# Kernel tuning notes

Measured on AMD Instinct MI355X. Metric: run time of the kernel, lower is better.

## Reference

```python
import jax, jax.numpy as jnp
import numpy as np
from jax import lax

N, L, C_IN, NOISE_C, COMP, NC = 256, 512, 514, 112, 16, 2
MAIN_IN = NOISE_C + COMP  # 128
FEAT = NC * 4 * L         # 4096

def _conv1d(x, w, b, pad):
    # x [N,C,L], w [O,I,K]
    y = lax.conv_general_dilated(x, w, (1,), [(pad, pad)], dimension_numbers=('NCH', 'OIH', 'NCH'))
    return y + b[None, :, None]

def _bn(x, g, b):
    # BatchNorm1d, training mode: biased batch stats over (N, L)
    m = x.mean(axis=(0, 2), keepdims=True)
    v = x.var(axis=(0, 2), keepdims=True)
    return (x - m) * lax.rsqrt(v + 1e-5) * g[None, :, None] + b[None, :, None]

def _lrelu(x):
    return jnp.where(x >= 0, x, 0.2 * x)

def _pos_encode(length, dim):
    j = np.arange(dim)
    div = 1.0 / np.power(10000.0, 2 * (j[:, None] // 2) / dim)   # [dim,1]
    ang = np.arange(length)[None, :] * div                       # [dim,length]
    ang = np.where((j % 2 == 0)[:, None], np.sin(ang), np.cos(ang))
    return jnp.asarray(ang[None], jnp.float32)                   # [1,dim,length]

def _assemble(circle_prob, slider_prob):
    # Vectorized run-length label expansion equivalent to the per-sample python while-loop.
    # circle_prob [N, L/2, 2], slider_prob [N, L/4, 2] -> [N, L, 3]
    n, B = slider_prob.shape[0], slider_prob.shape[1]
    c = jnp.argmax(circle_prob, -1)
    s = jnp.argmax(slider_prob, -1)
    zc = jnp.zeros(circle_prob.shape[:-1] + (1,), circle_prob.dtype)
    zs = jnp.zeros(slider_prob.shape[:-1] + (1,), slider_prob.dtype)
    cp3 = jnp.concatenate([circle_prob, zc], -1)                                   # insert 0 at class 2
    sp3 = jnp.concatenate([slider_prob[..., :1], zs, slider_prob[..., 1:]], -1)    # insert 0 at class 1
    pad100 = jnp.array([1., 0., 0.], cp3.dtype)
    pad001 = jnp.array([0., 0., 1.], cp3.dtype)
    bidx = jnp.arange(B)[None, :]
    # slider-body blocks: slider run continues and not cut by sequence end
    body = (s == 1) & (bidx < B - 1)
    prev_body = jnp.concatenate([jnp.zeros((n, 1), bool), body[:, :-1]], 1)
    # tail block ends a slider run (either run stops, or boundary block)
    tail = ((s == 1) & (bidx == B - 1)) | ((s == 0) & prev_body)
    # circle emission for each half-step: prob row if predicted circle else pad
    cr0 = jnp.where((c == 1)[..., None], cp3, pad100).reshape(n, B, 2, 3)
    bodyE = body[..., None]
    row0 = jnp.where((body | tail)[..., None], sp3, cr0[:, :, 0, :])
    row1 = jnp.where(bodyE, pad001, pad100)
    row2 = jnp.where(bodyE, pad001, cr0[:, :, 1, :])
    row3 = jnp.where(bodyE, pad001, pad100)
    return jnp.stack([row0, row1, row2, row3], 2).reshape(n, 4 * B, 3)

def _forward(noise, cond_data, gumbel_u, ext_w1, ext_b1, ext_w2, ext_b2, ext_bn_g, ext_bn_b,
             m_w1, m_b1, m_w2, m_b2, m_bn_g, m_bn_b, lin_w, lin_b, circ_w, circ_b, slid_w, slid_b):
    # FeatureExtractor
    x = cond_data.transpose(0, 2, 1)                      # [N, 514, L]
    x = _lrelu(_conv1d(x, ext_w1, ext_b1, 0))             # [N, 32, L]
    cond = _bn(_conv1d(x, ext_w2, ext_b2, 1), ext_bn_g, ext_bn_b)  # [N, 16, L]
    gen_in = jnp.concatenate([cond, noise.transpose(0, 2, 1)], 1) + _pos_encode(L, MAIN_IN)  # [N,128,L]
    h = _lrelu(_conv1d(gen_in, m_w1, m_b1, 3))            # [N, 32, L]
    h = _lrelu(_bn(_conv1d(h, m_w2, m_b2, 1), m_bn_g, m_bn_b))     # [N, 8, L]
    flat = _lrelu(h.reshape(h.shape[0], -1) @ lin_w + lin_b)       # [N, 4096]
    circle_prob = (flat @ circ_w + circ_b).reshape(-1, L // 2, NC)
    slider_prob = (flat @ slid_w + slid_b).reshape(-1, L // 4, NC)
    out = _assemble(circle_prob, slider_prob)             # [N, L, 3]
    # gumbel_softmax(hard=True, tau=1)
    g = -jnp.log(-jnp.log(gumbel_u + 1e-10) + 1e-10)
    logits = out + g
    y_soft = jax.nn.softmax(logits, -1)
    y_hard = jax.nn.one_hot(jnp.argmax(logits, -1), 3, dtype=y_soft.dtype)
    gen_out = y_hard + y_soft - lax.stop_gradient(y_soft)
    return gen_out, cond

def setup_inputs() -> dict:
    key = jax.random.key(0)
    ks = jax.random.split(key, 12)
    def rn(k, shape, fan_in):
        return jax.random.normal(k, shape, jnp.float32) * (1.0 / fan_in) ** 0.5
    return {
        'noise': jax.random.normal(ks[0], (N, L, NOISE_C), jnp.float32),
        'cond_data': jax.random.normal(ks[1], (N, L, C_IN), jnp.float32),
        'gumbel_u': jax.random.uniform(ks[2], (N, L, 3), jnp.float32),
        'ext_w1': rn(ks[3], (C_IN // 16, C_IN, 1), C_IN), 'ext_b1': jnp.zeros(C_IN // 16),
        'ext_w2': rn(ks[4], (COMP, C_IN // 16, 3), 3 * (C_IN // 16)), 'ext_b2': jnp.zeros(COMP),
        'ext_bn_g': jnp.ones(COMP), 'ext_bn_b': jnp.zeros(COMP),
        'm_w1': rn(ks[5], (NC * 16, MAIN_IN, 7), 7 * MAIN_IN), 'm_b1': jnp.zeros(NC * 16),
        'm_w2': rn(ks[6], (NC * 4, NC * 16, 3), 3 * NC * 16), 'm_b2': jnp.zeros(NC * 4),
        'm_bn_g': jnp.ones(NC * 4), 'm_bn_b': jnp.zeros(NC * 4),
        'lin_w': rn(ks[7], (FEAT, FEAT), FEAT), 'lin_b': jnp.zeros(FEAT),
        'circ_w': rn(ks[8], (FEAT, NC * L // 2), FEAT), 'circ_b': jnp.zeros(NC * L // 2),
        'slid_w': rn(ks[9], (FEAT, NC * L // 4), FEAT), 'slid_b': jnp.zeros(NC * L // 4),
    }

def reference(noise, cond_data, gumbel_u, ext_w1, ext_b1, ext_w2, ext_b2, ext_bn_g, ext_bn_b,
              m_w1, m_b1, m_w2, m_b2, m_bn_g, m_bn_b, lin_w, lin_b, circ_w, circ_b, slid_w, slid_b):
    return _forward(noise, cond_data, gumbel_u, ext_w1, ext_b1, ext_w2, ext_b2, ext_bn_g, ext_bn_b,
                    m_w1, m_b1, m_w2, m_b2, m_bn_g, m_bn_b, lin_w, lin_b, circ_w, circ_b, slid_w, slid_b)
```

## Files before the change

kernel.cpp:

```cpp
#include <hip/hip_runtime.h>
#include <math.h>

#define NB 256
#define LL 512
#define CIN 514

__device__ __forceinline__ float lrelu(float x) { return x >= 0.f ? x : 0.2f * x; }

__global__ __launch_bounds__(256) void k_pos(float* __restrict__ pos) {
    int idx = blockIdx.x * 256 + threadIdx.x;
    int c = idx >> 9, l = idx & 511;
    double e = (double)(2 * (c >> 1)) / 128.0;
    double dv = 1.0 / pow(10000.0, e);
    double a = (double)l * dv;
    pos[idx] = (float)((c & 1) ? cos(a) : sin(a));
}

__global__ __launch_bounds__(256) void k_posconv(const float* __restrict__ POS, const float* __restrict__ W,
                                                 const float* __restrict__ bias, float* __restrict__ PC) {
    const int t = threadIdx.x;
    const int o = blockIdx.x >> 4, l0 = (blockIdx.x & 15) * 32;
    const int l = l0 + (t & 31), cs = t >> 5;
    float acc = 0.f;
    for (int ci = 0; ci < 16; ++ci) {
        int c = cs * 16 + ci;
        float wv[7];
#pragma unroll
        for (int k = 0; k < 7; ++k) wv[k] = W[o * 896 + c * 7 + k];
#pragma unroll
        for (int k = 0; k < 7; ++k) {
            int gl = l + k - 3;
            if (gl >= 0 && gl < LL) acc += wv[k] * POS[c * LL + gl];
        }
    }
    __shared__ float red[8][33];
    red[cs][t & 31] = acc;
    __syncthreads();
    if (cs == 0) {
        float s = bias[o];
#pragma unroll
        for (int j = 0; j < 8; ++j) s += red[j][t & 31];
        PC[o * LL + l0 + (t & 31)] = s;
    }
}

__global__ __launch_bounds__(256) void k_conv1(const float* __restrict__ X, const float* __restrict__ W,
                                               float* __restrict__ P0, float* __restrict__ P1) {
    __shared__ __align__(16) float As[16][524];
    __shared__ __align__(16) float Bs[16][36];
    const int t = threadIdx.x;
    const int n = blockIdx.x >> 1, z = blockIdx.x & 1;
    const int kbase = z * 256;
    const int nch = z ? 17 : 16;
    const int tl = t & 63, to = t >> 6;
    const size_t rowbase = (size_t)n * 512 * CIN;

    float acc[8][8];
#pragma unroll
    for (int oi = 0; oi < 8; ++oi)
#pragma unroll
        for (int p = 0; p < 8; ++p) acc[oi][p] = 0.f;

    float2 pf[16];
    float2 pfb;

    {
        const int kb = kbase;
#pragma unroll
        for (int ps = 0; ps < 16; ++ps) {
            int idx = ps * 256 + t;
            int pos = idx >> 3, kp = idx & 7;
            int gk = kb + kp * 2;
            float2 v = {0.f, 0.f};
            if (gk + 1 < CIN) v = *(const float2*)(X + rowbase + (size_t)pos * CIN + gk);
            else if (gk < CIN) v.x = X[rowbase + (size_t)pos * CIN + gk];
            pf[ps] = v;
        }
        {
            int o = t >> 3, kp = t & 7;
            int gk = kb + kp * 2;
            float2 v = {0.f, 0.f};
            if (gk + 1 < CIN) v = *(const float2*)(W + (size_t)o * CIN + gk);
            else if (gk < CIN) v.x = W[(size_t)o * CIN + gk];
            pfb = v;
        }
#pragma unroll
        for (int ps = 0; ps < 16; ++ps) {
            int idx = ps * 256 + t;
            int pos = idx >> 3, kp = idx & 7;
            As[kp * 2][pos] = pf[ps].x;
            As[kp * 2 + 1][pos] = pf[ps].y;
        }
        {
            int o = t >> 3, kp = t & 7;
            Bs[kp * 2][o] = pfb.x;
            Bs[kp * 2 + 1][o] = pfb.y;
        }
    }
    __syncthreads();

    for (int c = 0; c < nch; ++c) {
        if (c + 1 < nch) {
            const int kb = kbase + (c + 1) * 16;
#pragma unroll
            for (int ps = 0; ps < 16; ++ps) {
                int idx = ps * 256 + t;
                int pos = idx >> 3, kp = idx & 7;
                int gk = kb + kp * 2;
                float2 v = {0.f, 0.f};
                if (gk + 1 < CIN) v = *(const float2*)(X + rowbase + (size_t)pos * CIN + gk);
                else if (gk < CIN) v.x = X[rowbase + (size_t)pos * CIN + gk];
                pf[ps] = v;
            }
            int o = t >> 3, kp = t & 7;
            int gk = kb + kp * 2;
            float2 v = {0.f, 0.f};
            if (gk + 1 < CIN) v = *(const float2*)(W + (size_t)o * CIN + gk);
            else if (gk < CIN) v.x = W[(size_t)o * CIN + gk];
            pfb = v;
        }
#pragma unroll
        for (int kk = 0; kk < 16; ++kk) {
            float4 aL = *(const float4*)&As[kk][tl * 4];
            float4 aH = *(const float4*)&As[kk][256 + tl * 4];
            float4 b0 = *(const float4*)&Bs[kk][to * 8];
            float4 b1 = *(const float4*)&Bs[kk][to * 8 + 4];
            float av[8] = {aL.x, aL.y, aL.z, aL.w, aH.x, aH.y, aH.z, aH.w};
            float bv[8] = {b0.x, b0.y, b0.z, b0.w, b1.x, b1.y, b1.z, b1.w};
#pragma unroll
            for (int oi = 0; oi < 8; ++oi)
#pragma unroll
                for (int p = 0; p < 8; ++p) acc[oi][p] += av[p] * bv[oi];
        }
        __syncthreads();
        if (c + 1 < nch) {
#pragma unroll
            for (int ps = 0; ps < 16; ++ps) {
                int idx = ps * 256 + t;
                int pos = idx >> 3, kp = idx & 7;
                As[kp * 2][pos] = pf[ps].x;
                As[kp * 2 + 1][pos] = pf[ps].y;
            }
            int o = t >> 3, kp = t & 7;
            Bs[kp * 2][o] = pfb.x;
            Bs[kp * 2 + 1][o] = pfb.y;
        }
        __syncthreads();
    }

    float* P = z ? P1 : P0;
#pragma unroll
    for (int oi = 0; oi < 8; ++oi) {
        int o = to * 8 + oi;
        float4 v0 = {acc[oi][0], acc[oi][1], acc[oi][2], acc[oi][3]};
        float4 v1 = {acc[oi][4], acc[oi][5], acc[oi][6], acc[oi][7]};
        *(float4*)(P + ((size_t)n * 32 + o) * LL + tl * 4) = v0;
        *(float4*)(P + ((size_t)n * 32 + o) * LL + 256 + tl * 4) = v1;
    }
}

__global__ __launch_bounds__(256) void k_conv2(const float* __restrict__ P0, const float* __restrict__ P1,
                                               const float* __restrict__ b1, const float* __restrict__ W,
                                               const float* __restrict__ bias, float* __restrict__ out) {
    __shared__ __align__(16) float Xs[32][264];
    __shared__ __align__(16) float Ws[16][32][4];
    const int t = threadIdx.x;
    const int n = blockIdx.x >> 1, l0 = (blockIdx.x & 1) * 256;
    for (int idx = t; idx < 32 * 258; idx += 256) {
        int i = idx / 258, j = idx % 258;
        int gl = l0 - 1 + j;
        float v = 0.f;
        if (gl >= 0 && gl < LL) {
            size_t off = ((size_t)n * 32 + i) * LL + gl;
            v = lrelu(P0[off] + P1[off] + b1[i]);
        }
        Xs[i][j] = v;
    }
    for (int idx = t; idx < 1536; idx += 256) {
        int o = idx / 96, r = idx % 96;
        Ws[o][r / 3][r % 3] = W[idx];
    }
    __syncthreads();
    const int tx = t & 31, ty = t >> 5;
    float acc[2][8];
#pragma unroll
    for (int q = 0; q < 2; ++q)
#pragma unroll
        for (int p = 0; p < 8; ++p) acc[q][p] = 0.f;
    for (int i = 0; i < 32; ++i) {
        float4 a0 = *(const float4*)&Xs[i][tx*8];
        float4 a1 = *(const float4*)&Xs[i][tx*8+4];
        float4 a2 = *(const float4*)&Xs[i][tx*8+8];
        float a[12] = {a0.x,a0.y,a0.z,a0.w,a1.x,a1.y,a1.z,a1.w,a2.x,a2.y,a2.z,a2.w};
#pragma unroll
        for (int q = 0; q < 2; ++q) {
            float4 b = *(const float4*)&Ws[ty*2+q][i][0];
#pragma unroll
            for (int p = 0; p < 8; ++p)
                acc[q][p] += a[p]*b.x + a[p+1]*b.y + a[p+2]*b.z;
        }
    }
#pragma unroll
    for (int q = 0; q < 2; ++q) {
        int o = ty*2+q; float bb = bias[o];
#pragma unroll
        for (int h = 0; h < 2; ++h) {
            float4 v;
            v.x = acc[q][h*4+0] + bb; v.y = acc[q][h*4+1] + bb;
            v.z = acc[q][h*4+2] + bb; v.w = acc[q][h*4+3] + bb;
            *(float4*)(out + ((size_t)n*16 + o)*LL + l0 + tx*8 + h*4) = v;
        }
    }
}

__global__ __launch_bounds__(256) void k_redstats(const float* __restrict__ src, int C, float* __restrict__ part) {
    const int ch = blockIdx.x, sl = blockIdx.y, t = threadIdx.x;
    float s = 0.f, q = 0.f;
    for (int i = t; i < 4096; i += 256) {
        int n = sl*8 + (i >> 9), l = i & 511;
        float v = src[((size_t)n*C + ch)*LL + l];
        s += v; q += v*v;
    }
    __shared__ float rs[256], rq[256];
    rs[t] = s; rq[t] = q;
    __syncthreads();
    for (int off = 128; off > 0; off >>= 1) {
        if (t < off) { rs[t] += rs[t+off]; rq[t] += rq[t+off]; }
        __syncthreads();
    }
    if (t == 0) { part[(ch*32+sl)*2] = rs[0]; part[(ch*32+sl)*2+1] = rq[0]; }
}

__global__ void k_bnfinal(const float* __restrict__ part, const float* __restrict__ g,
                          const float* __restrict__ b, int C, float* __restrict__ ss) {
    int ch = threadIdx.x;
    if (ch >= C) return;
    float s = 0.f, q = 0.f;
    for (int j = 0; j < 32; ++j) { s += part[(ch*32 + j)*2]; q += part[(ch*32 + j)*2 + 1]; }
    float mean = s * (1.f/131072.f);
    float var = q * (1.f/131072.f) - mean*mean;
    float sc = g[ch] / sqrtf(var + 1e-5f);
    ss[ch] = sc;
    ss[C + ch] = b[ch] - mean * sc;
}

__global__ __launch_bounds__(256) void k_bnapply(const float* __restrict__ src, const float* __restrict__ ss,
        int C, float* __restrict__ dst, int act, int total4) {
    int i4 = blockIdx.x * 256 + threadIdx.x;
    if (i4 >= total4) return;
    int i = i4 << 2;
    int ch = (i >> 9) % C;
    float sc = ss[ch], sh = ss[C + ch];
    float4 v = reinterpret_cast<const float4*>(src)[i4];
    v.x = v.x*sc + sh; v.y = v.y*sc + sh; v.z = v.z*sc + sh; v.w = v.w*sc + sh;
    if (act) { v.x = lrelu(v.x); v.y = lrelu(v.y); v.z = lrelu(v.z); v.w = lrelu(v.w); }
    reinterpret_cast<float4*>(dst)[i4] = v;
}

__global__ __launch_bounds__(256) void k_mconv1(const float* __restrict__ C16, const float* __restrict__ NZ,
        const float* __restrict__ PC, const float* __restrict__ W,
        float* __restrict__ out0, float* __restrict__ out1) {
    __shared__ __align__(16) float Gs[16][264];
    __shared__ __align__(16) float Ws[32][16][8];
    const int t = threadIdx.x;
    const int n = blockIdx.x >> 2, l0 = ((blockIdx.x >> 1) & 1) * 256, z = blockIdx.x & 1;
    const int tx = t & 31, ty = t >> 5;
    float acc[4][8];
#pragma unroll
    for (int q = 0; q < 4; ++q)
#pragma unroll
        for (int p = 0; p < 8; ++p) acc[q][p] = 0.f;

    for (int cc = 0; cc < 4; ++cc) {
        const int ctg = z * 4 + cc;
        if (cc) __syncthreads();
        if (ctg == 0) {
            for (int idx = t; idx < 16*262; idx += 256) {
                int c = idx / 262, j = idx - c * 262;
                int gl = l0 - 3 + j;
                float v = 0.f;
                if (gl >= 0 && gl < LL) v = C16[((size_t)n*16 + c)*LL + gl];
                Gs[c][j] = v;
            }
        } else {
            int nc0 = ctg * 16 - 16;
            for (int idx = t; idx < 16*262; idx += 256) {
                int c = idx & 15, j = idx >> 4;
                int gl = l0 - 3 + j;
                float v = 0.f;
                if (gl >= 0 && gl < LL) v = NZ[((size_t)n*LL + gl)*112 + nc0 + c];
                Gs[c][j] = v;
            }
        }
        for (int idx = t; idx < 32*112; idx += 256) {
            int o = idx / 112, r = idx % 112;
            Ws[o][r / 7][r % 7] = W[(size_t)o*896 + ctg*112 + r];
        }
        __syncthreads();
        for (int ci = 0; ci < 16; ++ci) {
            float4 a0 = *(const float4*)&Gs[ci][tx*4];
            float4 a1 = *(const float4*)&Gs[ci][tx*4+4];
            float4 a2 = *(const float4*)&Gs[ci][tx*4+8];
            float4 a3 = *(const float4*)&Gs[ci][128+tx*4];
            float4 a4 = *(const float4*)&Gs[ci][128+tx*4+4];
            float4 a5 = *(const float4*)&Gs[ci][128+tx*4+8];
            float aA[12] = {a0.x,a0.y,a0.z,a0.w,a1.x,a1.y,a1.z,a1.w,a2.x,a2.y,a2.z,a2.w};
            float aB[12] = {a3.x,a3.y,a3.z,a3.w,a4.x,a4.y,a4.z,a4.w,a5.x,a5.y,a5.z,a5.w};
#pragma unroll
            for (int q = 0; q < 4; ++q) {
                float4 b0 = *(const float4*)&Ws[ty*4+q][ci][0];
                float4 b1 = *(const float4*)&Ws[ty*4+q][ci][4];
                float b[7] = {b0.x,b0.y,b0.z,b0.w,b1.x,b1.y,b1.z};
#pragma unroll
                for (int p = 0; p < 4; ++p) {
#pragma unroll
                    for (int k = 0; k < 7; ++k) {
                        acc[q][p]   += aA[p+k]*b[k];
                        acc[q][4+p] += aB[p+k]*b[k];
                    }
                }
            }
        }
    }
    float* out = z ? out1 : out0;
#pragma unroll
    for (int q = 0; q < 4; ++q) {
        int o = ty*4 + q;
        float4 p0 = {0.f,0.f,0.f,0.f}, p1 = {0.f,0.f,0.f,0.f};
        if (z == 0) {
            p0 = *(const float4*)(PC + o*LL + l0 + tx*4);
            p1 = *(const float4*)(PC + o*LL + l0 + 128 + tx*4);
        }
        float4 v0 = {acc[q][0]+p0.x, acc[q][1]+p0.y, acc[q][2]+p0.z, acc[q][3]+p0.w};
        float4 v1 = {acc[q][4]+p1.x, acc[q][5]+p1.y, acc[q][6]+p1.z, acc[q][7]+p1.w};
        *(float4*)(out + ((size_t)n*32 + o)*LL + l0 + tx*4) = v0;
        *(float4*)(out + ((size_t)n*32 + o)*LL + l0 + 128 + tx*4) = v1;
    }
}

__global__ __launch_bounds__(256) void k_mconv2(const float* __restrict__ P0, const float* __restrict__ P1,
        const float* __restrict__ W, const float* __restrict__ bias, float* __restrict__ out) {
    __shared__ __align__(16) float Xs[32][264];
    __shared__ __align__(16) float Ws[8][32][4];
    const int t = threadIdx.x;
    const int n = blockIdx.x >> 1, l0 = (blockIdx.x & 1) * 256;
    for (int idx = t; idx < 32 * 258; idx += 256) {
        int i = idx / 258, j = idx % 258;
        int gl = l0 - 1 + j;
        float v = 0.f;
        if (gl >= 0 && gl < LL) {
            size_t off = ((size_t)n * 32 + i) * LL + gl;
            v = lrelu(P0[off] + P1[off]);
        }
        Xs[i][j] = v;
    }
    for (int idx = t; idx < 768; idx += 256) {
        int o = idx / 96, r = idx % 96;
        Ws[o][r / 3][r % 3] = W[idx];
    }
    __syncthreads();
    const int tx = t & 31, ty = t >> 5;
    float acc[8];
#pragma unroll
    for (int p = 0; p < 8; ++p) acc[p] = 0.f;
    for (int i = 0; i < 32; ++i) {
        float4 a0 = *(const float4*)&Xs[i][tx*8];
        float4 a1 = *(const float4*)&Xs[i][tx*8+4];
        float4 a2 = *(const float4*)&Xs[i][tx*8+8];
        float a[12] = {a0.x,a0.y,a0.z,a0.w,a1.x,a1.y,a1.z,a1.w,a2.x,a2.y,a2.z,a2.w};
        float4 b = *(const float4*)&Ws[ty][i][0];
#pragma unroll
        for (int p = 0; p < 8; ++p)
            acc[p] += a[p]*b.x + a[p+1]*b.y + a[p+2]*b.z;
    }
    float bb = bias[ty];
#pragma unroll
    for (int h = 0; h < 2; ++h) {
        float4 v;
        v.x = acc[h*4+0] + bb; v.y = acc[h*4+1] + bb;
        v.z = acc[h*4+2] + bb; v.w = acc[h*4+3] + bb;
        *(float4*)(out + ((size_t)n*8 + ty)*LL + l0 + tx*8 + h*4) = v;
    }
}

__global__ __launch_bounds__(256) void k_lin(const float* __restrict__ A, const float* __restrict__ B,
                                             float* __restrict__ part) {
    __shared__ __align__(16) float As[32][36];
    __shared__ __align__(16) float Bs[32][132];
    const int t = threadIdx.x;
    const int m0 = blockIdx.x * 32, f0 = blockIdx.y * 128, z = blockIdx.z;
    const int tm = t & 7, tf = t >> 3;
    const int mi = t >> 3, kq = t & 7;
    float acc[4][4];
#pragma unroll
    for (int pm = 0; pm < 4; ++pm)
#pragma unroll
        for (int pf = 0; pf < 4; ++pf) acc[pm][pf] = 0.f;
    for (int k0 = z * 2048; k0 < z * 2048 + 2048; k0 += 32) {
        float4 av = *(const float4*)(A + (size_t)(m0 + mi) * 4096 + k0 + kq * 4);
        As[kq*4+0][mi] = av.x; As[kq*4+1][mi] = av.y; As[kq*4+2][mi] = av.z; As[kq*4+3][mi] = av.w;
#pragma unroll
        for (int pass = 0; pass < 4; ++pass) {
            int fi = pass * 32 + kq * 4;
            *(float4*)&Bs[mi][fi] = *(const float4*)(B + (size_t)(k0 + mi) * 4096 + f0 + fi);
        }
        __syncthreads();
#pragma unroll 8
        for (int kk = 0; kk < 32; ++kk) {
            float4 a = *(const float4*)&As[kk][tm * 4];
            float4 b = *(const float4*)&Bs[kk][tf * 4];
            float avv[4] = {a.x,a.y,a.z,a.w};
            float bvv[4] = {b.x,b.y,b.z,b.w};
#pragma unroll
            for (int pm = 0; pm < 4; ++pm)
#pragma unroll
                for (int pf = 0; pf < 4; ++pf) acc[pm][pf] += avv[pm]*bvv[pf];
        }
        __syncthreads();
    }
#pragma unroll
    for (int pm = 0; pm < 4; ++pm) {
        float4 v = {acc[pm][0], acc[pm][1], acc[pm][2], acc[pm][3]};
        *(float4*)(part + ((size_t)z * 256 + m0 + tm * 4 + pm) * 4096 + f0 + tf * 4) = v;
    }
}

__global__ __launch_bounds__(256) void k_linred(const float* __restrict__ part, const float* __restrict__ bias,
        float* __restrict__ out) {
    int i4 = blockIdx.x*256 + threadIdx.x;
    int i = i4 << 2;
    int f = i & 4095;
    float4 a = ((const float4*)part)[i4];
    float4 c = ((const float4*)(part + 1048576))[i4];
    float4 bb = *(const float4*)(bias + f);
    float4 r;
    r.x = lrelu(a.x + c.x + bb.x);
    r.y = lrelu(a.y + c.y + bb.y);
    r.z = lrelu(a.z + c.z + bb.z);
    r.w = lrelu(a.w + c.w + bb.w);
    ((float4*)out)[i4] = r;
}

__global__ __launch_bounds__(256) void k_heads(const float* __restrict__ A, const float* __restrict__ CW,
        const float* __restrict__ SW, float* __restrict__ part) {
    __shared__ __align__(16) float As[32][36];
    __shared__ __align__(16) float Bs[32][132];
    const int t = threadIdx.x;
    const int m0 = blockIdx.x * 32, f0 = blockIdx.y * 128, z = blockIdx.z;
    const float* B; int ldb, fb;
    if (f0 < 512) { B = CW; ldb = 512; fb = f0; } else { B = SW; ldb = 256; fb = f0 - 512; }
    const int tm = t & 7, tf = t >> 3;
    const int mi = t >> 3, kq = t & 7;
    float acc[4][4];
#pragma unroll
    for (int pm = 0; pm < 4; ++pm)
#pragma unroll
        for (int pf = 0; pf < 4; ++pf) acc[pm][pf] = 0.f;
    for (int k0 = z * 512; k0 < z * 512 + 512; k0 += 32) {
        float4 av = *(const float4*)(A + (size_t)(m0 + mi) * 4096 + k0 + kq * 4);
        As[kq*4+0][mi] = av.x; As[kq*4+1][mi] = av.y; As[kq*4+2][mi] = av.z; As[kq*4+3][mi] = av.w;
#pragma unroll
        for (int pass = 0; pass < 4; ++pass) {
            int fi = pass * 32 + kq * 4;
            *(float4*)&Bs[mi][fi] = *(const float4*)(B + (size_t)(k0 + mi) * ldb + fb + fi);
        }
        __syncthreads();
#pragma unroll 8
        for (int kk = 0; kk < 32; ++kk) {
            float4 a = *(const float4*)&As[kk][tm * 4];
            float4 b = *(const float4*)&Bs[kk][tf * 4];
            float avv[4] = {a.x,a.y,a.z,a.w};
            float bvv[4] = {b.x,b.y,b.z,b.w};
#pragma unroll
            for (int pm = 0; pm < 4; ++pm)
#pragma unroll
                for (int pf = 0; pf < 4; ++pf) acc[pm][pf] += avv[pm]*bvv[pf];
        }
        __syncthreads();
    }
#pragma unroll
    for (int pm = 0; pm < 4; ++pm) {
        float4 v = {acc[pm][0], acc[pm][1], acc[pm][2], acc[pm][3]};
        *(float4*)(part + ((size_t)z * 256 + m0 + tm * 4 + pm) * 768 + f0 + tf * 4) = v;
    }
}

__global__ __launch_bounds__(256) void k_headred(const float* __restrict__ part, const float* __restrict__ cb,
        const float* __restrict__ sb, float* __restrict__ circ, float* __restrict__ slid) {
    int i4 = blockIdx.x * 256 + threadIdx.x;
    int i = i4 << 2;
    int n = i / 768, f = i % 768;
    float4 s = {0.f,0.f,0.f,0.f};
#pragma unroll
    for (int ks = 0; ks < 8; ++ks) {
        float4 p = *(const float4*)(part + ((size_t)ks*256 + n)*768 + f);
        s.x += p.x; s.y += p.y; s.z += p.z; s.w += p.w;
    }
    if (f < 512) {
        float4 bb = *(const float4*)(cb + f);
        s.x += bb.x; s.y += bb.y; s.z += bb.z; s.w += bb.w;
        *(float4*)(circ + (size_t)n*512 + f) = s;
    } else {
        float4 bb = *(const float4*)(sb + f - 512);
        s.x += bb.x; s.y += bb.y; s.z += bb.z; s.w += bb.w;
        *(float4*)(slid + (size_t)n*256 + f - 512) = s;
    }
}

__global__ __launch_bounds__(128) void k_assemble(const float* __restrict__ circ, const float* __restrict__ slid,
        const float* __restrict__ gum, float* __restrict__ out) {
    const int n = blockIdx.x;
    const int b = threadIdx.x;
    const float* sp = slid + (size_t)n * 256;
    const float* cp = circ + (size_t)n * 512;
    float sl0 = sp[2*b], sl1 = sp[2*b+1];
    int s = sl1 > sl0 ? 1 : 0;
    int prevb = 0;
    if (b > 0) prevb = (sp[2*b-1] > sp[2*b-2]) ? 1 : 0;
    bool body = (s == 1) && (b < 127);
    bool tail = ((s == 1) && (b == 127)) || ((s == 0) && (prevb == 1));
    float c0a = cp[4*b], c0b = cp[4*b+1], c1a = cp[4*b+2], c1b = cp[4*b+3];
    bool cA = c0b > c0a, cB = c1b > c1a;
    float rows[4][3];
    if (body || tail)      { rows[0][0]=sl0; rows[0][1]=0.f; rows[0][2]=sl1; }
    else if (cA)           { rows[0][0]=c0a; rows[0][1]=c0b; rows[0][2]=0.f; }
    else                   { rows[0][0]=1.f; rows[0][1]=0.f; rows[0][2]=0.f; }
    if (body)              { rows[1][0]=0.f; rows[1][1]=0.f; rows[1][2]=1.f; }
    else                   { rows[1][0]=1.f; rows[1][1]=0.f; rows[1][2]=0.f; }
    if (body)              { rows[2][0]=0.f; rows[2][1]=0.f; rows[2][2]=1.f; }
    else if (cB)           { rows[2][0]=c1a; rows[2][1]=c1b; rows[2][2]=0.f; }
    else                   { rows[2][0]=1.f; rows[2][1]=0.f; rows[2][2]=0.f; }
    rows[3][0]=rows[1][0]; rows[3][1]=rows[1][1]; rows[3][2]=rows[1][2];
#pragma unroll
    for (int r = 0; r < 4; ++r) {
        int l = 4*b + r;
        const float* u = gum + ((size_t)n*512 + l)*3;
        float g0 = -logf(-logf(u[0]+1e-10f)+1e-10f);
        float g1 = -logf(-logf(u[1]+1e-10f)+1e-10f);
        float g2 = -logf(-logf(u[2]+1e-10f)+1e-10f);
        float t0 = rows[r][0]+g0, t1 = rows[r][1]+g1, t2 = rows[r][2]+g2;
        int am = 0; float mv = t0;
        if (t1 > mv) { am = 1; mv = t1; }
        if (t2 > mv) { am = 2; mv = t2; }
        float e0 = expf(t0-mv), e1 = expf(t1-mv), e2 = expf(t2-mv);
        float ssum = e0+e1+e2;
        float y0 = e0/ssum, y1 = e1/ssum, y2 = e2/ssum;
        float* o = out + ((size_t)n*512 + l)*3;
        o[0] = ((am==0?1.f:0.f) + y0) - y0;
        o[1] = ((am==1?1.f:0.f) + y1) - y1;
        o[2] = ((am==2?1.f:0.f) + y2) - y2;
    }
}

extern "C" void kernel_launch(void* const* d_in, const int* in_sizes, int n_in,
                              void* d_out, int out_size, void* d_ws, size_t ws_size,
                              hipStream_t stream) {
    const float* noise   = (const float*)d_in[0];
    const float* cond    = (const float*)d_in[1];
    const float* gumbel  = (const float*)d_in[2];
    const float* ext_w1  = (const float*)d_in[3];
    const float* ext_b1  = (const float*)d_in[4];
    const float* ext_w2  = (const float*)d_in[5];
    const float* ext_b2  = (const float*)d_in[6];
    const float* ext_bng = (const float*)d_in[7];
    const float* ext_bnb = (const float*)d_in[8];
    const float* m_w1    = (const float*)d_in[9];
    const float* m_b1    = (const float*)d_in[10];
    const float* m_w2    = (const float*)d_in[11];
    const float* m_b2    = (const float*)d_in[12];
    const float* m_bng   = (const float*)d_in[13];
    const float* m_bnb   = (const float*)d_in[14];
    const float* lin_w   = (const float*)d_in[15];
    const float* lin_b   = (const float*)d_in[16];
    const float* circ_w  = (const float*)d_in[17];
    const float* circ_b  = (const float*)d_in[18];
    const float* slid_w  = (const float*)d_in[19];
    const float* slid_b  = (const float*)d_in[20];

    float* genout  = (float*)d_out;
    float* condout = (float*)d_out + 256*512*3;

    float* w     = (float*)d_ws;
    float* x1    = w;
    float* y2    = x1 + 4194304;
    float* posb  = y2 + 2097152;
    float* circ  = posb + 65536;
    float* slid  = circ + 131072;
    float* flatB = slid + 65536;
    float* partL = flatB + 1048576;
    float* partH = partL + 2097152;
    float* stats = partH + 1572864;
    float* pc    = stats + 4096;
    float* buf1  = flatB;

    k_pos<<<256, 256, 0, stream>>>(posb);
    k_posconv<<<512, 256, 0, stream>>>(posb, m_w1, m_b1, pc);
    k_conv1<<<512, 256, 0, stream>>>(cond, ext_w1, x1, buf1);
    k_conv2<<<512, 256, 0, stream>>>(x1, buf1, ext_b1, ext_w2, ext_b2, y2);
    k_redstats<<<dim3(16,32), 256, 0, stream>>>(y2, 16, stats);
    k_bnfinal<<<1, 64, 0, stream>>>(stats, ext_bng, ext_bnb, 16, stats + 2048);
    k_bnapply<<<2048, 256, 0, stream>>>(y2, stats + 2048, 16, condout, 0, 524288);
    k_mconv1<<<1024, 256, 0, stream>>>(condout, noise, pc, m_w1, x1, buf1);
    k_mconv2<<<512, 256, 0, stream>>>(x1, buf1, m_w2, m_b2, y2);
    k_redstats<<<dim3(8,32), 256, 0, stream>>>(y2, 8, stats);
    k_bnfinal<<<1, 64, 0, stream>>>(stats, m_bng, m_bnb, 8, stats + 2048 + 64);
    k_bnapply<<<1024, 256, 0, stream>>>(y2, stats + 2048 + 64, 8, y2, 1, 262144);
    k_lin<<<dim3(8,32,2), 256, 0, stream>>>(y2, lin_w, partL);
    k_linred<<<1024, 256, 0, stream>>>(partL, lin_b, flatB);
    k_heads<<<dim3(8,6,8), 256, 0, stream>>>(flatB, circ_w, slid_w, partH);
    k_headred<<<192, 256, 0, stream>>>(partH, circ_b, slid_b, circ, slid);
    k_assemble<<<256, 128, 0, stream>>>(circ, slid, gumbel, genout);
}
```

Measured before the change: 550.1 us.

## Retile linear GEMM to 64x64 blocks with register prefetch and swizzled block order

The 4096x4096 linear layer GEMM moves from 32x128 tiles to square 64x64 tiles, which gives better balance between A and B reuse per block. The next K-slice is prefetched into registers while the current tile is computed, so global load latency overlaps with the FMAs. A 1D grid with remapped block indices groups blocks that share B columns to improve L2 locality. The cost is higher register pressure and two barriers per iteration.

```diff
diff --git a/kernel.cpp b/kernel.cpp
--- a/kernel.cpp
+++ b/kernel.cpp
@@ -385,43 +385,79 @@
 
 __global__ __launch_bounds__(256) void k_lin(const float* __restrict__ A, const float* __restrict__ B,
                                              float* __restrict__ part) {
-    __shared__ __align__(16) float As[32][36];
-    __shared__ __align__(16) float Bs[32][132];
+    __shared__ __align__(16) float As[32][68];
+    __shared__ __align__(16) float Bs[32][68];
     const int t = threadIdx.x;
-    const int m0 = blockIdx.x * 32, f0 = blockIdx.y * 128, z = blockIdx.z;
-    const int tm = t & 7, tf = t >> 3;
-    const int mi = t >> 3, kq = t & 7;
+    const int bid = blockIdx.x;
+    const int x = bid & 7, j = bid >> 3;
+    const int f0 = (x * 8 + (j & 7)) * 64;
+    const int m0 = ((j >> 3) & 3) * 64;
+    const int z = j >> 5;
+    const int lane = t & 63, wv = t >> 6;
+    const int smi = t & 63, skq = t >> 6;
+    const int ski = t >> 3, sf4 = t & 7;
+    const int k0base = z * 2048;
+
+    const int ar = wv * 16 + ((lane >> 4) << 2);
+    const int br = (lane & 15) << 2;
+
     float acc[4][4];
 #pragma unroll
-    for (int pm = 0; pm < 4; ++pm)
-#pragma unroll
-        for (int pf = 0; pf < 4; ++pf) acc[pm][pf] = 0.f;
-    for (int k0 = z * 2048; k0 < z * 2048 + 2048; k0 += 32) {
-        float4 av = *(const float4*)(A + (size_t)(m0 + mi) * 4096 + k0 + kq * 4);
-        As[kq*4+0][mi] = av.x; As[kq*4+1][mi] = av.y; As[kq*4+2][mi] = av.z; As[kq*4+3][mi] = av.w;
-#pragma unroll
-        for (int pass = 0; pass < 4; ++pass) {
-            int fi = pass * 32 + kq * 4;
-            *(float4*)&Bs[mi][fi] = *(const float4*)(B + (size_t)(k0 + mi) * 4096 + f0 + fi);
-        }
-        __syncthreads();
-#pragma unroll 8
+    for (int i = 0; i < 4; ++i)
+#pragma unroll
+        for (int q = 0; q < 4; ++q) acc[i][q] = 0.f;
+
+    float4 pa0, pa1, pb0, pb1;
+    {
+        const float* pA = A + (size_t)(m0 + smi) * 4096 + k0base;
+        pa0 = *(const float4*)(pA + skq * 4);
+        pa1 = *(const float4*)(pA + skq * 4 + 16);
+        const float* pB = B + (size_t)(k0base + ski) * 4096 + f0;
+        pb0 = *(const float4*)(pB + sf4 * 4);
+        pb1 = *(const float4*)(pB + sf4 * 4 + 32);
+        As[skq*4+0][smi] = pa0.x; As[skq*4+1][smi] = pa0.y; As[skq*4+2][smi] = pa0.z; As[skq*4+3][smi] = pa0.w;
+        As[skq*4+16][smi] = pa1.x; As[skq*4+17][smi] = pa1.y; As[skq*4+18][smi] = pa1.z; As[skq*4+19][smi] = pa1.w;
+        *(float4*)&Bs[ski][sf4*4] = pb0;
+        *(float4*)&Bs[ski][sf4*4+32] = pb1;
+    }
+    __syncthreads();
+
+    for (int it = 0; it < 64; ++it) {
+        if (it + 1 < 64) {
+            const int k0 = k0base + (it + 1) * 32;
+            const float* pA = A + (size_t)(m0 + smi) * 4096 + k0;
+            pa0 = *(const float4*)(pA + skq * 4);
+            pa1 = *(const float4*)(pA + skq * 4 + 16);
+            const float* pB = B + (size_t)(k0 + ski) * 4096 + f0;
+            pb0 = *(const float4*)(pB + sf4 * 4);
+            pb1 = *(const float4*)(pB + sf4 * 4 + 32);
+        }
+#pragma unroll
         for (int kk = 0; kk < 32; ++kk) {
-            float4 a = *(const float4*)&As[kk][tm * 4];
-            float4 b = *(const float4*)&Bs[kk][tf * 4];
-            float avv[4] = {a.x,a.y,a.z,a.w};
-            float bvv[4] = {b.x,b.y,b.z,b.w};
-#pragma unroll
-            for (int pm = 0; pm < 4; ++pm)
-#pragma unroll
-                for (int pf = 0; pf < 4; ++pf) acc[pm][pf] += avv[pm]*bvv[pf];
-        }
-        __syncthreads();
-    }
-#pragma unroll
-    for (int pm = 0; pm < 4; ++pm) {
-        float4 v = {acc[pm][0], acc[pm][1], acc[pm][2], acc[pm][3]};
-        *(float4*)(part + ((size_t)z * 256 + m0 + tm * 4 + pm) * 4096 + f0 + tf * 4) = v;
+            float4 a = *(const float4*)&As[kk][ar];
+            float4 b = *(const float4*)&Bs[kk][br];
+            float av[4] = {a.x, a.y, a.z, a.w};
+            float bv[4] = {b.x, b.y, b.z, b.w};
+#pragma unroll
+            for (int i = 0; i < 4; ++i)
+#pragma unroll
+                for (int q = 0; q < 4; ++q) acc[i][q] += av[i] * bv[q];
+        }
+        __syncthreads();
+        if (it + 1 < 64) {
+            As[skq*4+0][smi] = pa0.x; As[skq*4+1][smi] = pa0.y; As[skq*4+2][smi] = pa0.z; As[skq*4+3][smi] = pa0.w;
+            As[skq*4+16][smi] = pa1.x; As[skq*4+17][smi] = pa1.y; As[skq*4+18][smi] = pa1.z; As[skq*4+19][smi] = pa1.w;
+            *(float4*)&Bs[ski][sf4*4] = pb0;
+            *(float4*)&Bs[ski][sf4*4+32] = pb1;
+        }
+        __syncthreads();
+    }
+
+#pragma unroll
+    for (int i = 0; i < 4; ++i) {
+        int m = m0 + ar + i;
+        float4 v = {acc[i][0], acc[i][1], acc[i][2], acc[i][3]};
+        *(float4*)(part + ((size_t)z * 256 + m) * 4096 + f0 + br) = v;
     }
 }
 
@@ -605,7 +641,7 @@
     k_redstats<<<dim3(8,32), 256, 0, stream>>>(y2, 8, stats);
     k_bnfinal<<<1, 64, 0, stream>>>(stats, m_bng, m_bnb, 8, stats + 2048 + 64);
     k_bnapply<<<1024, 256, 0, stream>>>(y2, stats + 2048 + 64, 8, y2, 1, 262144);
-    k_lin<<<dim3(8,32,2), 256, 0, stream>>>(y2, lin_w, partL);
+    k_lin<<<512, 256, 0, stream>>>(y2, lin_w, partL);
     k_linred<<<1024, 256, 0, stream>>>(partL, lin_b, flatB);
     k_heads<<<dim3(8,6,8), 256, 0, stream>>>(flatB, circ_w, slid_w, partH);
     k_headred<<<192, 256, 0, stream>>>(partH, circ_b, slid_b, circ, slid);
```

Measured after the change: 579.6 us. 5.4% more time.
